# Kernel optimization log

Measured on AMD Instinct MI355X. Metric: run time of the kernel, lower is better.

## Reference

```python
import jax, jax.numpy as jnp
import numpy as np

B, TQ, TK = 4, 256, 256
Q, K, H = 256, 256, 256


def setup_inputs() -> dict:
    key = jax.random.key(0)
    ks = jax.random.split(key, 10)
    s = 0.05
    return {
        "queries": jax.random.normal(ks[0], (B, TQ, Q), dtype=jnp.float32),
        "keys": jax.random.normal(ks[1], (B, TK, K), dtype=jnp.float32),
        # lengths in [T//2, T] so no fully-masked query rows (torch would NaN there too)
        "query_lengths": jax.random.randint(ks[2], (B,), TQ // 2, TQ + 1),
        "key_lengths": jax.random.randint(ks[3], (B,), TK // 2, TK + 1),
        # nn.Linear(Q+K, H): weight applied as x @ W1; torch concat order is [keys, queries]
        "W1": jax.random.normal(ks[4], (K + Q, H), dtype=jnp.float32) * s,
        "b1": jax.random.normal(ks[5], (H,), dtype=jnp.float32) * s,
        "W2": jax.random.normal(ks[6], (H, H), dtype=jnp.float32) * s,
        "b2": jax.random.normal(ks[7], (H,), dtype=jnp.float32) * s,
        "W3": jax.random.normal(ks[8], (H, 1), dtype=jnp.float32) * s,
        "b3": jax.random.normal(ks[9], (1,), dtype=jnp.float32) * s,
    }


def reference(queries, keys, query_lengths, key_lengths, W1, b1, W2, b2, W3, b3):
    Bn, Tq, Qd = queries.shape
    Tk, Kd = keys.shape[1], keys.shape[2]
    # Split the first linear: concat([keys, queries]) @ W1 == keys@W1[:K] + queries@W1[K:]
    kh = jnp.einsum("bkd,dh->bkh", keys, W1[:Kd])      # [B,Tk,H]
    qh = jnp.einsum("bqd,dh->bqh", queries, W1[Kd:])   # [B,Tq,H]
    h = jax.nn.relu(qh[:, :, None, :] + kh[:, None, :, :] + b1)  # [B,Tq,Tk,H]
    h = jax.nn.relu(jnp.einsum("bqkh,hg->bqkg", h, W2) + b2)     # [B,Tq,Tk,H]
    scores = jnp.einsum("bqkh,h->bqk", h, W3[:, 0]) + b3[0]       # [B,Tq,Tk]
    # mask True where position is padding (query OR key out of range)
    mask = (jnp.arange(Tq)[None, :, None] >= query_lengths[:, None, None]) | (
        jnp.arange(Tk)[None, None, :] >= key_lengths[:, None, None]
    )
    scores = jnp.where(mask, -1e30, scores)
    probs = jax.nn.softmax(scores, axis=-1)
    probs = jnp.where(mask, 0.0, probs)
    return jnp.einsum("bqk,bkd->bqd", probs, keys)  # [B,Tq,K]
```

## Files before the change

### kernel.cpp

```cpp
#include <hip/hip_runtime.h>
#include <cstdint>

#define BATCH 4
#define TQ 256
#define TK 256
#define DIM 256
#define HD 256

typedef _Float16 f16x8 __attribute__((ext_vector_type(8)));
typedef float f32x4 __attribute__((ext_vector_type(4)));

union U4H8 { uint4 u; f16x8 v; };

__device__ __forceinline__ unsigned short f2h(float f) {
    _Float16 h = (_Float16)f;
    unsigned short u;
    __builtin_memcpy(&u, &h, 2);
    return u;
}

__device__ __forceinline__ uint32_t pk2h(float a, float b) {
    auto r = __builtin_amdgcn_cvt_pkrtz(a, b);
    uint32_t w;
    __builtin_memcpy(&w, &r, 4);
    return w;
}

__global__ __launch_bounds__(256) void prep_all(
    const float* __restrict__ queries, const float* __restrict__ keys,
    const float* __restrict__ W1, const float* __restrict__ b1,
    const float* __restrict__ W2,
    float* __restrict__ qh, float* __restrict__ kh,
    unsigned short* __restrict__ W2T) {
    int i = blockIdx.x;
    int t = threadIdx.x;
    if (i >= 256) {
        __shared__ float tile[32][33];
        int bi = i - 256;
        int tx = t & 31, ty = t >> 5;
        int tc = (bi & 7) * 32, tn = (bi >> 3) * 32;
#pragma unroll
        for (int r = 0; r < 4; ++r)
            tile[ty + r * 8][tx] = W2[(tc + ty + r * 8) * HD + tn + tx];
        __syncthreads();
#pragma unroll
        for (int r = 0; r < 4; ++r)
            W2T[(tn + ty + r * 8) * HD + tc + tx] = f2h(tile[tx][ty + r * 8]);
        return;
    }
    bool isQ = i < 128;
    int r0 = (i & 127) * 8;
    const float* X = isQ ? queries : keys;
    const float* W = W1 + (isQ ? DIM * HD : 0);
    float* O = isQ ? qh : kh;
    __shared__ float xs[8][DIM];
#pragma unroll
    for (int r = 0; r < 8; ++r) xs[r][t] = X[(r0 + r) * DIM + t];
    __syncthreads();
    float acc[8] = {0.f, 0.f, 0.f, 0.f, 0.f, 0.f, 0.f, 0.f};
#pragma unroll 4
    for (int d = 0; d < DIM; ++d) {
        float w = W[d * HD + t];
#pragma unroll
        for (int r = 0; r < 8; ++r) acc[r] = fmaf(xs[r][d], w, acc[r]);
    }
    float bias = isQ ? b1[t] : 0.f;
#pragma unroll
    for (int r = 0; r < 8; ++r) O[(r0 + r) * HD + t] = acc[r] + bias;
}

__global__ __launch_bounds__(256, 2) void mlp_attn(
    const float* __restrict__ qh, const float* __restrict__ kh,
    const unsigned short* __restrict__ W2T,
    const float* __restrict__ b2, const float* __restrict__ W3,
    const float* __restrict__ keys,
    const int* __restrict__ qlens, const int* __restrict__ klens,
    float* __restrict__ out) {
    int bid = blockIdx.x;
    int b = bid >> 8;
    int q = bid & 255;
    int t = threadIdx.x;
    float* orow = out + (b * TQ + q) * DIM;
    if (q >= qlens[b]) { orow[t] = 0.f; return; }
    int klen = klens[b];
    int nch = (klen + 63) >> 6;

    __shared__ uint4 Afrag[2][8][4][64];
    __shared__ float srow[TK];
    __shared__ float red[8];

    int wid = t >> 6, lane = t & 63;
    int col = lane & 15, quad = lane >> 4;

    int nb = wid * 64;
    uint4 bfr[4][8];
    float b2v[4], w3v[4];
#pragma unroll
    for (int nt = 0; nt < 4; ++nt) {
        int n = nb + nt * 16 + col;
        const uint4* r = (const uint4*)(W2T + n * HD) + quad;
#pragma unroll
        for (int s = 0; s < 8; ++s) bfr[nt][s] = r[s * 4];
        b2v[nt] = b2[n];
        w3v[nt] = W3[n];
    }

    int p = t >> 2, j8 = t & 3;
    const float* qrow = qh + (b * TQ + q) * HD + j8 * 8;
    const float* kbase = kh + b * TK * HD + j8 * 8;
    int aoff = ((p >> 4) << 6) | (p & 15) | (j8 << 4);

    auto stage = [&](int c, int d) {
        const float* krow = kbase + (c * 64 + p) * HD;
        uint4* aslot = &Afrag[d][0][0][0] + aoff;
#pragma unroll
        for (int s = 0; s < 8; ++s) {
            const float4 k0 = *(const float4*)(krow + s * 32);
            const float4 k1 = *(const float4*)(krow + s * 32 + 4);
            const float4 q0 = *(const float4*)(qrow + s * 32);
            const float4 q1 = *(const float4*)(qrow + s * 32 + 4);
            uint4 w;
            w.x = pk2h(fmaxf(k0.x + q0.x, 0.f), fmaxf(k0.y + q0.y, 0.f));
            w.y = pk2h(fmaxf(k0.z + q0.z, 0.f), fmaxf(k0.w + q0.w, 0.f));
            w.z = pk2h(fmaxf(k1.x + q1.x, 0.f), fmaxf(k1.y + q1.y, 0.f));
            w.w = pk2h(fmaxf(k1.z + q1.z, 0.f), fmaxf(k1.w + q1.w, 0.f));
            aslot[s * 256] = w;
        }
    };

    srow[t] = 0.f;
    stage(0, 0);
    __syncthreads();

    for (int c = 0; c < nch; ++c) {
        int cur = c & 1;
        if (c + 1 < nch) stage(c + 1, cur ^ 1);

        f32x4 acc[4][4] = {};
#pragma unroll
        for (int s = 0; s < 8; ++s) {
#pragma unroll
            for (int mt = 0; mt < 4; ++mt) {
                U4H8 au;
                au.u = Afrag[cur][s][mt][lane];
#pragma unroll
                for (int nt = 0; nt < 4; ++nt) {
                    U4H8 bu;
                    bu.u = bfr[nt][s];
                    acc[mt][nt] = __builtin_amdgcn_mfma_f32_16x16x32_f16(
                        au.v, bu.v, acc[mt][nt], 0, 0, 0);
                }
            }
        }

#pragma unroll
        for (int mt = 0; mt < 4; ++mt) {
            float part[4];
#pragma unroll
            for (int r = 0; r < 4; ++r) {
                float pa = 0.f;
#pragma unroll
                for (int nt = 0; nt < 4; ++nt)
                    pa = fmaf(fmaxf(acc[mt][nt][r] + b2v[nt], 0.f), w3v[nt], pa);
                part[r] = pa;
            }
#pragma unroll
            for (int off = 1; off < 16; off <<= 1)
#pragma unroll
                for (int r = 0; r < 4; ++r)
                    part[r] += __shfl_xor(part[r], off, 64);
            if (col == 0)
#pragma unroll
                for (int r = 0; r < 4; ++r)
                    atomicAdd(&srow[c * 64 + mt * 16 + quad * 4 + r], part[r]);
        }
        __syncthreads();
    }

    float s = (t < klen) ? srow[t] : -3.4e38f;
    float m = s;
#pragma unroll
    for (int off = 1; off < 64; off <<= 1) m = fmaxf(m, __shfl_xor(m, off, 64));
    if (lane == 0) red[wid] = m;
    __syncthreads();
    m = fmaxf(fmaxf(red[0], red[1]), fmaxf(red[2], red[3]));
    float e = (t < klen) ? __expf(s - m) : 0.f;
    float sum = e;
#pragma unroll
    for (int off = 1; off < 64; off <<= 1) sum += __shfl_xor(sum, off, 64);
    if (lane == 0) red[4 + wid] = sum;
    __syncthreads();
    float denom = red[4] + red[5] + red[6] + red[7];
    srow[t] = e / denom;
    __syncthreads();

    float acc = 0.f;
    const float* kp = keys + b * TK * DIM + t;
#pragma unroll 8
    for (int k = 0; k < klen; ++k) acc = fmaf(srow[k], kp[k * DIM], acc);
    orow[t] = acc;
}

extern "C" void kernel_launch(void* const* d_in, const int* in_sizes, int n_in,
                              void* d_out, int out_size, void* d_ws, size_t ws_size,
                              hipStream_t stream) {
    (void)in_sizes; (void)n_in; (void)out_size; (void)ws_size;
    const float* queries = (const float*)d_in[0];
    const float* keys    = (const float*)d_in[1];
    const int*   qlens   = (const int*)d_in[2];
    const int*   klens   = (const int*)d_in[3];
    const float* W1      = (const float*)d_in[4];
    const float* b1      = (const float*)d_in[5];
    const float* W2      = (const float*)d_in[6];
    const float* b2      = (const float*)d_in[7];
    const float* W3      = (const float*)d_in[8];
    float* out = (float*)d_out;

    float* qh = (float*)d_ws;
    float* kh = qh + BATCH * TQ * HD;
    unsigned short* W2T = (unsigned short*)(kh + BATCH * TK * HD);

    prep_all<<<320, 256, 0, stream>>>(queries, keys, W1, b1, W2, qh, kh, W2T);
    mlp_attn<<<BATCH * TQ, 256, 0, stream>>>(
        qh, kh, W2T, b2, W3, keys, qlens, klens, out);
}
```

Baseline: 150.0 us.

## Halve register-resident W2 fragments and stream the rest from global per chunk

```diff
diff --git a/kernel.cpp b/kernel.cpp
--- a/kernel.cpp
+++ b/kernel.cpp
@@ -50,19 +50,16 @@
     }
     bool isQ = i < 128;
     int r0 = (i & 127) * 8;
-    const float* X = isQ ? queries : keys;
+    const float* X = (isQ ? queries : keys) + r0 * DIM;
     const float* W = W1 + (isQ ? DIM * HD : 0);
     float* O = isQ ? qh : kh;
-    __shared__ float xs[8][DIM];
-#pragma unroll
-    for (int r = 0; r < 8; ++r) xs[r][t] = X[(r0 + r) * DIM + t];
-    __syncthreads();
     float acc[8] = {0.f, 0.f, 0.f, 0.f, 0.f, 0.f, 0.f, 0.f};
 #pragma unroll 4
     for (int d = 0; d < DIM; ++d) {
         float w = W[d * HD + t];
 #pragma unroll
-        for (int r = 0; r < 8; ++r) acc[r] = fmaf(xs[r][d], w, acc[r]);
+        for (int r = 0; r < 8; ++r)
+            acc[r] = fmaf(X[r * DIM + d], w, acc[r]);
     }
     float bias = isQ ? b1[t] : 0.f;
 #pragma unroll
@@ -93,27 +90,27 @@
     int col = lane & 15, quad = lane >> 4;
 
     int nb = wid * 64;
-    uint4 bfr[4][8];
+    const uint4* w2r[4];
+    uint4 bfr0[4][4];
     float b2v[4], w3v[4];
 #pragma unroll
     for (int nt = 0; nt < 4; ++nt) {
         int n = nb + nt * 16 + col;
-        const uint4* r = (const uint4*)(W2T + n * HD) + quad;
-#pragma unroll
-        for (int s = 0; s < 8; ++s) bfr[nt][s] = r[s * 4];
+        w2r[nt] = (const uint4*)(W2T + n * HD) + quad;
+#pragma unroll
+        for (int s = 0; s < 4; ++s) bfr0[nt][s] = w2r[nt][s * 4];
         b2v[nt] = b2[n];
         w3v[nt] = W3[n];
     }
 
-    int p = t >> 2, j8 = t & 3;
-    const float* qrow = qh + (b * TQ + q) * HD + j8 * 8;
-    const float* kbase = kh + b * TK * HD + j8 * 8;
-    int aoff = ((p >> 4) << 6) | (p & 15) | (j8 << 4);
+    int p = (wid << 4) | col;
+    const float* qrow = qh + (b * TQ + q) * HD + quad * 8;
+    const float* kbase = kh + (b * TK) * HD + quad * 8;
 
     auto stage = [&](int c, int d) {
         const float* krow = kbase + (c * 64 + p) * HD;
-        uint4* aslot = &Afrag[d][0][0][0] + aoff;
-#pragma unroll
+        uint4* dst = &Afrag[d][0][wid][lane];
+#pragma unroll 2
         for (int s = 0; s < 8; ++s) {
             const float4 k0 = *(const float4*)(krow + s * 32);
             const float4 k1 = *(const float4*)(krow + s * 32 + 4);
@@ -124,7 +121,7 @@
             w.y = pk2h(fmaxf(k0.z + q0.z, 0.f), fmaxf(k0.w + q0.w, 0.f));
             w.z = pk2h(fmaxf(k1.x + q1.x, 0.f), fmaxf(k1.y + q1.y, 0.f));
             w.w = pk2h(fmaxf(k1.z + q1.z, 0.f), fmaxf(k1.w + q1.w, 0.f));
-            aslot[s * 256] = w;
+            dst[s * 256] = w;
         }
     };
 
@@ -134,11 +131,10 @@
 
     for (int c = 0; c < nch; ++c) {
         int cur = c & 1;
-        if (c + 1 < nch) stage(c + 1, cur ^ 1);
-
         f32x4 acc[4][4] = {};
-#pragma unroll
-        for (int s = 0; s < 8; ++s) {
+
+#pragma unroll
+        for (int s = 0; s < 4; ++s) {
 #pragma unroll
             for (int mt = 0; mt < 4; ++mt) {
                 U4H8 au;
@@ -146,12 +142,39 @@
 #pragma unroll
                 for (int nt = 0; nt < 4; ++nt) {
                     U4H8 bu;
-                    bu.u = bfr[nt][s];
+                    bu.u = bfr0[nt][s];
                     acc[mt][nt] = __builtin_amdgcn_mfma_f32_16x16x32_f16(
                         au.v, bu.v, acc[mt][nt], 0, 0, 0);
                 }
             }
         }
+
+        uint4 bst[2][4];
+#pragma unroll
+        for (int nt = 0; nt < 4; ++nt) bst[0][nt] = w2r[nt][16];
+#pragma unroll
+        for (int s = 4; s < 8; ++s) {
+            int pp = (s - 4) & 1;
+            if (s < 7) {
+#pragma unroll
+                for (int nt = 0; nt < 4; ++nt)
+                    bst[pp ^ 1][nt] = w2r[nt][(s + 1) * 4];
+            }
+#pragma unroll
+            for (int mt = 0; mt < 4; ++mt) {
+                U4H8 au;
+                au.u = Afrag[cur][s][mt][lane];
+#pragma unroll
+                for (int nt = 0; nt < 4; ++nt) {
+                    U4H8 bu;
+                    bu.u = bst[pp][nt];
+                    acc[mt][nt] = __builtin_amdgcn_mfma_f32_16x16x32_f16(
+                        au.v, bu.v, acc[mt][nt], 0, 0, 0);
+                }
+            }
+        }
+
+        if (c + 1 < nch) stage(c + 1, cur ^ 1);
 
 #pragma unroll
         for (int mt = 0; mt < 4; ++mt) {
```

New measurement: 159.7 us. 1.06x slower.
